# Kernel tuning notes

Hardware: AMD Instinct MI355X
Metric: run time of the kernel (lower is better)

## Reference

```python
import jax, jax.numpy as jnp
import numpy as np

# Static configuration (values of input_spatial_shapes are compile-time constants,
# mirroring how Deformable DETR fixes the FPN level sizes per image resolution).
SPATIAL_SHAPES = [(128, 128), (64, 64), (32, 32), (16, 16)]
N_HEADS = 8
N_LEVELS = 4
N_POINTS = 4
D_MODEL = 256
HEAD_DIM = D_MODEL // N_HEADS  # 32


def setup_inputs() -> dict:
    key = jax.random.key(0)
    ks = jax.random.split(key, 12)
    n = 1
    len_in = sum(h * w for h, w in SPATIAL_SHAPES)  # 21760
    len_q = len_in
    s = 0.02
    inp = {
        "query": jax.random.normal(ks[0], (n, len_q, D_MODEL), jnp.float32),
        "reference_points": jax.random.uniform(ks[1], (n, len_q, N_LEVELS, 2), jnp.float32),
        "input_flatten": jax.random.normal(ks[2], (n, len_in, D_MODEL), jnp.float32),
        "input_spatial_shapes": jnp.array(SPATIAL_SHAPES, jnp.int32),
        "input_level_start_index": jnp.array(
            np.cumsum([0] + [h * w for h, w in SPATIAL_SHAPES[:-1]]), jnp.int32
        ),
        # learned parameters (nn.Linear stores weight as [out, in])
        "W_off": jax.random.normal(ks[3], (N_HEADS * N_LEVELS * N_POINTS * 2, D_MODEL), jnp.float32) * s,
        "b_off": jax.random.normal(ks[4], (N_HEADS * N_LEVELS * N_POINTS * 2,), jnp.float32) * 0.5,
        "W_attn": jax.random.normal(ks[5], (N_HEADS * N_LEVELS * N_POINTS, D_MODEL), jnp.float32) * s,
        "b_attn": jnp.zeros((N_HEADS * N_LEVELS * N_POINTS,), jnp.float32),
        "W_val": jax.random.normal(ks[6], (D_MODEL, D_MODEL), jnp.float32) * s,
        "b_val": jnp.zeros((D_MODEL,), jnp.float32),
        "W_out": jax.random.normal(ks[7], (D_MODEL, D_MODEL), jnp.float32) * s,
        "b_out": jnp.zeros((D_MODEL,), jnp.float32),
    }
    return inp


def _bilinear_sample(img, grid, h, w):
    """torch F.grid_sample(mode='bilinear', padding_mode='zeros', align_corners=False).
    img:  [B, C, h, w]; grid: [B, Q, P, 2] in [-1, 1] -> returns [B, C, Q, P]."""
    B, C = img.shape[0], img.shape[1]
    Q, P = grid.shape[1], grid.shape[2]
    gx = (grid[..., 0] + 1.0) * (w * 0.5) - 0.5
    gy = (grid[..., 1] + 1.0) * (h * 0.5) - 0.5
    x0 = jnp.floor(gx)
    y0 = jnp.floor(gy)
    lx, ly = gx - x0, gy - y0
    x0i = x0.astype(jnp.int32)
    y0i = y0.astype(jnp.int32)
    flat = img.reshape(B, C, h * w)
    acc = jnp.zeros((B, C, Q * P), img.dtype)
    for dx, dy, wgt in (
        (0, 0, (1 - lx) * (1 - ly)),
        (1, 0, lx * (1 - ly)),
        (0, 1, (1 - lx) * ly),
        (1, 1, lx * ly),
    ):
        xi = x0i + dx
        yi = y0i + dy
        valid = (xi >= 0) & (xi < w) & (yi >= 0) & (yi < h)
        idx = (jnp.clip(yi, 0, h - 1) * w + jnp.clip(xi, 0, w - 1)).reshape(B, Q * P)
        vals = jnp.take_along_axis(flat, jnp.broadcast_to(idx[:, None, :], (B, C, Q * P)), axis=2)
        acc = acc + vals * (wgt * valid.astype(img.dtype)).reshape(B, 1, Q * P)
    return acc.reshape(B, C, Q, P)


def reference(query, reference_points, input_flatten, input_spatial_shapes,
              input_level_start_index, W_off, b_off, W_attn, b_attn,
              W_val, b_val, W_out, b_out):
    n, Q, C = query.shape
    # value projection
    value = input_flatten @ W_val.T + b_val                      # [n, Lin, C]
    value = value.reshape(n, -1, N_HEADS, HEAD_DIM)              # [n, Lin, H, D]
    # sampling offsets & attention weights from query
    off = (query @ W_off.T + b_off).reshape(n, Q, N_HEADS, N_LEVELS, N_POINTS, 2)
    aw = jax.nn.softmax(
        (query @ W_attn.T + b_attn).reshape(n, Q, N_HEADS, N_LEVELS * N_POINTS), axis=-1
    ).reshape(n, Q, N_HEADS, N_LEVELS, N_POINTS)
    # reference_points has last dim 2: normalize offsets by (w, h) per level
    norm = jnp.array([[w, h] for h, w in SPATIAL_SHAPES], jnp.float32)  # [L, 2]
    loc = reference_points[:, :, None, :, None, :] + off / norm[None, None, None, :, None, :]
    grids = 2.0 * loc - 1.0                                       # [n,Q,H,L,P,2]
    aw_t = aw.transpose(0, 2, 1, 3, 4).reshape(n * N_HEADS, 1, Q, N_LEVELS, N_POINTS)
    out = jnp.zeros((n * N_HEADS, HEAD_DIM, Q), query.dtype)
    start = 0
    for lvl, (h, w) in enumerate(SPATIAL_SHAPES):
        v = value[:, start:start + h * w]                         # [n, hw, H, D]
        start += h * w
        img = v.transpose(0, 2, 3, 1).reshape(n * N_HEADS, HEAD_DIM, h, w)
        g = grids[:, :, :, lvl].transpose(0, 2, 1, 3, 4).reshape(n * N_HEADS, Q, N_POINTS, 2)
        sampled = _bilinear_sample(img, g, h, w)                  # [nH, D, Q, P]
        out = out + (sampled * aw_t[:, :, :, lvl, :]).sum(-1)
    out = out.reshape(n, N_HEADS * HEAD_DIM, Q).transpose(0, 2, 1)  # [n, Q, C]
    return out @ W_out.T + b_out
```

## Files before the change

### kernel.cpp

```cpp
#include <hip/hip_runtime.h>
#include <math.h>

#define Q_TOTAL 21760
#define NBLK_M 340
#define QB 16
#define HEAD_IMG_BYTES 1392640

typedef _Float16     f16;
typedef short        s16x8 __attribute__((ext_vector_type(8)));
typedef f16          f16x8 __attribute__((ext_vector_type(8)));
typedef f16          f16x4 __attribute__((ext_vector_type(4)));
typedef f16          f16x2 __attribute__((ext_vector_type(2)));
typedef __bf16       bfv8  __attribute__((ext_vector_type(8)));
typedef float        f32x4 __attribute__((ext_vector_type(4)));
typedef float        f32x2 __attribute__((ext_vector_type(2)));
typedef unsigned int u32x4 __attribute__((ext_vector_type(4)));
typedef unsigned int u32x2 __attribute__((ext_vector_type(2)));

__device__ __forceinline__ s16x8 pack8(float4 a, float4 b) {
    bfv8 t;
    t[0] = (__bf16)a.x; t[1] = (__bf16)a.y; t[2] = (__bf16)a.z; t[3] = (__bf16)a.w;
    t[4] = (__bf16)b.x; t[5] = (__bf16)b.y; t[6] = (__bf16)b.z; t[7] = (__bf16)b.w;
    return __builtin_bit_cast(s16x8, t);
}

__global__ __launch_bounds__(256) void cvt_weights(
    const float* __restrict__ Woff, const float* __restrict__ Wattn,
    const float* __restrict__ Wval, const float* __restrict__ Wout,
    const float* __restrict__ boff, const float* __restrict__ battn,
    unsigned short* __restrict__ dst, float* __restrict__ bias_cat)
{
    if (blockIdx.x == 224) {
        const int t = threadIdx.x;
        bias_cat[t] = boff[t];
        if (t < 128) bias_cat[256 + t] = battn[t];
        return;
    }
    const int e = blockIdx.x * 1024 + threadIdx.x * 4;
    const float* src; int base;
    if (e < 65536)       { src = Woff;  base = 0; }
    else if (e < 98304)  { src = Wattn; base = 65536; }
    else if (e < 163840) { src = Wval;  base = 98304; }
    else                 { src = Wout;  base = 163840; }
    float4 v = *(const float4*)(src + (e - base));
    ushort4 o;
    o.x = __builtin_bit_cast(unsigned short, (__bf16)v.x);
    o.y = __builtin_bit_cast(unsigned short, (__bf16)v.y);
    o.z = __builtin_bit_cast(unsigned short, (__bf16)v.z);
    o.w = __builtin_bit_cast(unsigned short, (__bf16)v.w);
    *(ushort4*)(dst + e) = o;
}

template<bool A_BF16, int CMODE>
__global__ __launch_bounds__(256) void gemm_mfma(
    const void* __restrict__ Avoid,
    const unsigned short* __restrict__ W16,
    const float* __restrict__ bias,
    void* __restrict__ Cvoid,
    int ldc)
{
    constexpr int K = 256, BM = 64, BN = 128;
    constexpr int NB2 = BN / 2;
    constexpr int NF = NB2 / 16;
    __shared__ unsigned short As[BM * 32];
    __shared__ unsigned short Bs[BN * 32];

    const int tid  = threadIdx.x;
    const int lane = tid & 63;
    const int wv   = tid >> 6;
    const int wr   = wv >> 1, wc = wv & 1;
    const int rowBase = blockIdx.x * BM;
    const int colBase = blockIdx.y * BN;

    const int sr    = tid >> 2;
    const int skq   = (tid & 3) * 8;
    const int sslot = (tid & 3) * 16;

    f32x4 acc[2][NF];
#pragma unroll
    for (int i = 0; i < 2; i++)
#pragma unroll
        for (int j = 0; j < NF; j++) acc[i][j] = (f32x4){0.f, 0.f, 0.f, 0.f};

    const size_t arow = (size_t)(rowBase + sr) * K;

    for (int kt = 0; kt < K; kt += 32) {
        s16x8 aval;
        if constexpr (A_BF16) {
            const unsigned short* A16 = (const unsigned short*)Avoid;
            aval = *(const s16x8*)(A16 + arow + kt + skq);
        } else {
            const float* A32 = (const float*)Avoid;
            const float* p = A32 + arow + kt + skq;
            aval = pack8(*(const float4*)p, *(const float4*)(p + 4));
        }
        s16x8 bval[2];
#pragma unroll
        for (int c = 0; c < 2; c++) {
            const unsigned short* p = W16 + (size_t)(colBase + c * 64 + sr) * K + kt + skq;
            bval[c] = *(const s16x8*)p;
        }
        __syncthreads();
        *(s16x8*)(As + (((sr * 64 + sslot) ^ ((sr & 7) << 4)) >> 1)) = aval;
#pragma unroll
        for (int c = 0; c < 2; c++) {
            const int row = c * 64 + sr;
            *(s16x8*)(Bs + (((row * 64 + sslot) ^ ((row & 7) << 4)) >> 1)) = bval[c];
        }
        __syncthreads();
        s16x8 af[2];
#pragma unroll
        for (int mi = 0; mi < 2; mi++) {
            const int row = wr * 32 + mi * 16 + (lane & 15);
            af[mi] = *(const s16x8*)(As + (((row * 64 + (lane >> 4) * 16) ^ ((row & 7) << 4)) >> 1));
        }
#pragma unroll
        for (int ni = 0; ni < NF; ni++) {
            const int row = wc * NB2 + ni * 16 + (lane & 15);
            s16x8 bfrag = *(const s16x8*)(Bs + (((row * 64 + (lane >> 4) * 16) ^ ((row & 7) << 4)) >> 1));
#pragma unroll
            for (int mi = 0; mi < 2; mi++)
                acc[mi][ni] = __builtin_amdgcn_mfma_f32_16x16x32_bf16(af[mi], bfrag, acc[mi][ni], 0, 0, 0);
        }
    }

#pragma unroll
    for (int ni = 0; ni < NF; ni++) {
        const int col = colBase + wc * NB2 + ni * 16 + (lane & 15);
        const float bv = bias[col];
#pragma unroll
        for (int mi = 0; mi < 2; mi++) {
            const int r0 = rowBase + wr * 32 + mi * 16 + (lane >> 4) * 4;
#pragma unroll
            for (int j = 0; j < 4; j++) {
                const float v = acc[mi][ni][j] + bv;
                if constexpr (CMODE == 2) {
                    ((f16*)Cvoid)[((size_t)(col >> 5) * Q_TOTAL + (r0 + j)) * 32 + (col & 31)] = (f16)v;
                } else if constexpr (CMODE == 1) {
                    ((f16*)Cvoid)[(size_t)(r0 + j) * ldc + col] = (f16)v;
                } else {
                    ((float*)Cvoid)[(size_t)(r0 + j) * ldc + col] = v;
                }
            }
        }
    }
}

__global__ __launch_bounds__(256) void sample_kernel(
    const f16* __restrict__ value_t,
    const f16* __restrict__ offattn,
    const float* __restrict__ refpts,
    unsigned short* __restrict__ sampled)
{
    __shared__ __attribute__((aligned(16))) unsigned s_iw[32 * 132];

    const int tid   = threadIdx.x;
    const int qt    = blockIdx.x >> 2;
    const int hp    = blockIdx.x & 3;
    const int qbase = qt * QB;

    {
        const int q  = tid >> 4;
        const int h  = (tid >> 3) & 1;
        const int l  = (tid >> 1) & 3;
        const int ph = tid & 1;
        const int H  = hp * 2 + h;
        const int g  = tid >> 3;
        const f16* oa = offattn + (size_t)(qbase + q) * 384;

        f16x2 lgh = *(const f16x2*)(oa + 256 + H * 16 + l * 4 + ph * 2);
        const float lg0 = (float)lgh[0], lg1 = (float)lgh[1];
        float m = fmaxf(lg0, lg1);
        m = fmaxf(m, __shfl_xor(m, 1));
        m = fmaxf(m, __shfl_xor(m, 2));
        m = fmaxf(m, __shfl_xor(m, 4));
        float e0 = __expf(lg0 - m), e1 = __expf(lg1 - m);
        float s = e0 + e1;
        s += __shfl_xor(s, 1);
        s += __shfl_xor(s, 2);
        s += __shfl_xor(s, 4);
        const float inv = 1.f / s;
        const float aw2[2] = {e0 * inv, e1 * inv};

        f16x4 offh = *(const f16x4*)(oa + H * 32 + l * 8 + ph * 4);
        f32x2 rp = *(const f32x2*)(refpts + (size_t)(qbase + q) * 8 + l * 2);

        const int   SZ[4] = {128, 64, 32, 16};
        const int   ST[4] = {0, 16384, 20480, 21504};
        const int   W_ = SZ[l], START = ST[l];
        const float S = (float)W_;

        unsigned* dst = &s_iw[g * 132 + (l * 4 + ph * 2) * 8];
#pragma unroll
        for (int c = 0; c < 2; c++) {
            const float ox = (float)offh[c * 2], oy = (float)offh[c * 2 + 1];
            const float a = aw2[c];
            const float gx = fmaf(rp[0], S, ox) - 0.5f;
            const float gy = fmaf(rp[1], S, oy) - 0.5f;
            const float x0f = floorf(gx), y0f = floorf(gy);
            const float lx = gx - x0f, ly = gy - y0f;
            const int x0 = (int)x0f, y0 = (int)y0f;
            const int xs  = min(max(x0, 0), W_ - 2);
            const int sft = xs - x0;
            const float wx0 = (x0 >= 0 && x0 < W_) ? (1.f - lx) : 0.f;
            const float wx1 = (x0 + 1 >= 0 && x0 + 1 < W_) ? lx : 0.f;
            const float wxA = (sft == 0) ? wx0 : ((sft == 1) ? wx1 : 0.f);
            const float wxB = (sft == 0) ? wx1 : ((sft == -1) ? wx0 : 0.f);
            const int y1 = y0 + 1;
            const int y0c = min(max(y0, 0), W_ - 1);
            const int y1c = min(max(y1, 0), W_ - 1);
            const float wy0a = (((y0 >= 0) && (y0 < W_)) ? (1.f - ly) : 0.f) * a;
            const float wy1a = (((y1 >= 0) && (y1 < W_)) ? ly : 0.f) * a;
            const unsigned o0 = (unsigned)((START + y0c * W_ + xs) * 64);
            const unsigned o1 = (unsigned)((START + y1c * W_ + xs) * 64);
            u32x4 r0, r1;
            r0[0] = o0;      r0[1] = o1;
            r0[2] = __float_as_uint(wy0a * wxA);
            r0[3] = __float_as_uint(wy1a * wxA);
            r1[0] = o0 + 64; r1[1] = o1 + 64;
            r1[2] = __float_as_uint(wy0a * wxB);
            r1[3] = __float_as_uint(wy1a * wxB);
            *(u32x4*)(dst + c * 8)     = r0;
            *(u32x4*)(dst + c * 8 + 4) = r1;
        }
    }
    __syncthreads();

    {
        const int d8 = tid & 3;
        const int xc = (tid >> 2) & 1;
        const int g  = tid >> 3;
        const int q  = g >> 1;
        const int h  = g & 1;
        const int H  = hp * 2 + h;
        const unsigned vbase = (unsigned)(H * HEAD_IMG_BYTES) + (unsigned)(d8 * 16);
        const char* vt = (const char*)value_t;
        const unsigned* iw = &s_iw[g * 132 + xc * 4];

        float acc[8] = {0.f, 0.f, 0.f, 0.f, 0.f, 0.f, 0.f, 0.f};
#pragma unroll
        for (int half = 0; half < 2; half++) {
            u32x2 off[8];
#pragma unroll
            for (int p = 0; p < 8; p++)
                off[p] = *(const u32x2*)(iw + (half * 8 + p) * 8);
            f16x8 v0[8], v1[8];
#pragma unroll
            for (int p = 0; p < 8; p++) {
                v0[p] = *(const f16x8*)(vt + (size_t)(vbase + off[p][0]));
                v1[p] = *(const f16x8*)(vt + (size_t)(vbase + off[p][1]));
            }
#pragma unroll
            for (int p = 0; p < 8; p++) {
                const f32x2 w = *(const f32x2*)(iw + (half * 8 + p) * 8 + 2);
#pragma unroll
                for (int r = 0; r < 8; r++) {
                    acc[r] = fmaf((float)v0[p][r], w[0], acc[r]);
                    acc[r] = fmaf((float)v1[p][r], w[1], acc[r]);
                }
            }
        }
#pragma unroll
        for (int j = 0; j < 8; j++) acc[j] += __shfl_xor(acc[j], 4);

        if (xc == 0) {
            s16x8 o = pack8(make_float4(acc[0], acc[1], acc[2], acc[3]),
                            make_float4(acc[4], acc[5], acc[6], acc[7]));
            *(s16x8*)(sampled + (size_t)(qbase + q) * 256 + H * 32 + d8 * 8) = o;
        }
    }
}

extern "C" void kernel_launch(void* const* d_in, const int* in_sizes, int n_in,
                              void* d_out, int out_size, void* d_ws, size_t ws_size,
                              hipStream_t stream) {
    const float* query  = (const float*)d_in[0];
    const float* refpts = (const float*)d_in[1];
    const float* input_flatten = (const float*)d_in[2];
    const float* W_off  = (const float*)d_in[5];
    const float* b_off  = (const float*)d_in[6];
    const float* W_attn = (const float*)d_in[7];
    const float* b_attn = (const float*)d_in[8];
    const float* W_val  = (const float*)d_in[9];
    const float* b_val  = (const float*)d_in[10];
    const float* W_out  = (const float*)d_in[11];
    const float* b_out  = (const float*)d_in[12];
    float* out = (float*)d_out;

    char* ws = (char*)d_ws;
    f16*            value_t = (f16*)ws;
    f16*            offattn = (f16*)(ws + 11141120);
    unsigned short* sampled = (unsigned short*)(ws + 27852800);
    unsigned short* w16     = (unsigned short*)(ws + 38993920);
    float*          bias_cat= (float*)(ws + 39452672);
    unsigned short* w16_val  = w16 + 98304;
    unsigned short* w16_out  = w16 + 163840;

    cvt_weights<<<225, 256, 0, stream>>>(W_off, W_attn, W_val, W_out, b_off, b_attn, w16, bias_cat);

    gemm_mfma<false, 2><<<dim3(NBLK_M, 2), 256, 0, stream>>>(input_flatten, w16_val, b_val, value_t, 256);
    gemm_mfma<false, 1><<<dim3(NBLK_M, 3), 256, 0, stream>>>(query, w16, bias_cat, offattn, 384);
    sample_kernel<<<dim3((Q_TOTAL / QB) * 4), 256, 0, stream>>>(value_t, offattn, refpts, sampled);
    gemm_mfma<true, 0><<<dim3(NBLK_M, 2), 256, 0, stream>>>(sampled, w16_out, b_out, out, 256);
}
```

Measured before the change: 81.56 us.

## Fuse value and offset/attn projections into one launch, drop weight pre-conversion

Removes the separate weight-conversion kernel and instead converts fp32 weights to bf16 inline while loading each tile. The value projection and the offset/attention projection are merged into a single grid whose y-dimension selects the weight slab and output layout. Tiles grow from 64x128 to 128x128 with a 4x4 MFMA fragment grid per wave. This cuts two kernel launches and improves operand reuse, but every block now re-reads and re-converts fp32 weights, and the larger tiles raise register use and reduce the block count.

```diff
diff --git a/kernel.cpp b/kernel.cpp
--- a/kernel.cpp
+++ b/kernel.cpp
@@ -2,7 +2,6 @@
 #include <math.h>
 
 #define Q_TOTAL 21760
-#define NBLK_M 340
 #define QB 16
 #define HEAD_IMG_BYTES 1392640
 
@@ -24,124 +23,165 @@
     return __builtin_bit_cast(s16x8, t);
 }
 
-__global__ __launch_bounds__(256) void cvt_weights(
-    const float* __restrict__ Woff, const float* __restrict__ Wattn,
-    const float* __restrict__ Wval, const float* __restrict__ Wout,
-    const float* __restrict__ boff, const float* __restrict__ battn,
-    unsigned short* __restrict__ dst, float* __restrict__ bias_cat)
+__global__ __launch_bounds__(256) void gemm_fused(
+    const float* __restrict__ input_flatten,
+    const float* __restrict__ query,
+    const float* __restrict__ W_val,  const float* __restrict__ b_val,
+    const float* __restrict__ W_off,  const float* __restrict__ b_off,
+    const float* __restrict__ W_attn, const float* __restrict__ b_attn,
+    f16* __restrict__ value_t, f16* __restrict__ offattn)
 {
-    if (blockIdx.x == 224) {
-        const int t = threadIdx.x;
-        bias_cat[t] = boff[t];
-        if (t < 128) bias_cat[256 + t] = battn[t];
-        return;
-    }
-    const int e = blockIdx.x * 1024 + threadIdx.x * 4;
-    const float* src; int base;
-    if (e < 65536)       { src = Woff;  base = 0; }
-    else if (e < 98304)  { src = Wattn; base = 65536; }
-    else if (e < 163840) { src = Wval;  base = 98304; }
-    else                 { src = Wout;  base = 163840; }
-    float4 v = *(const float4*)(src + (e - base));
-    ushort4 o;
-    o.x = __builtin_bit_cast(unsigned short, (__bf16)v.x);
-    o.y = __builtin_bit_cast(unsigned short, (__bf16)v.y);
-    o.z = __builtin_bit_cast(unsigned short, (__bf16)v.z);
-    o.w = __builtin_bit_cast(unsigned short, (__bf16)v.w);
-    *(ushort4*)(dst + e) = o;
-}
-
-template<bool A_BF16, int CMODE>
-__global__ __launch_bounds__(256) void gemm_mfma(
-    const void* __restrict__ Avoid,
-    const unsigned short* __restrict__ W16,
-    const float* __restrict__ bias,
-    void* __restrict__ Cvoid,
-    int ldc)
-{
-    constexpr int K = 256, BM = 64, BN = 128;
-    constexpr int NB2 = BN / 2;
-    constexpr int NF = NB2 / 16;
-    __shared__ unsigned short As[BM * 32];
-    __shared__ unsigned short Bs[BN * 32];
+    constexpr int K = 256;
+    __shared__ unsigned short As[128 * 32];
+    __shared__ unsigned short Bs[128 * 32];
 
     const int tid  = threadIdx.x;
     const int lane = tid & 63;
     const int wv   = tid >> 6;
     const int wr   = wv >> 1, wc = wv & 1;
-    const int rowBase = blockIdx.x * BM;
-    const int colBase = blockIdx.y * BN;
-
-    const int sr    = tid >> 2;
-    const int skq   = (tid & 3) * 8;
-    const int sslot = (tid & 3) * 16;
-
-    f32x4 acc[2][NF];
-#pragma unroll
-    for (int i = 0; i < 2; i++)
-#pragma unroll
-        for (int j = 0; j < NF; j++) acc[i][j] = (f32x4){0.f, 0.f, 0.f, 0.f};
-
-    const size_t arow = (size_t)(rowBase + sr) * K;
+    const int rowBase = blockIdx.x * 128;
+    const int slab = blockIdx.y;
+
+    const float* A32; const float* Wf; const float* bias;
+    if (slab < 2)       { A32 = input_flatten; Wf = W_val + slab * 32768; bias = b_val + slab * 128; }
+    else if (slab == 2) { A32 = query;         Wf = W_off;                bias = b_off; }
+    else if (slab == 3) { A32 = query;         Wf = W_off + 32768;       bias = b_off + 128; }
+    else                { A32 = query;         Wf = W_attn;               bias = b_attn; }
+
+    const int sr  = tid >> 1;
+    const int sk0 = (tid & 1) * 16;
+    const int sby = (tid & 1) * 32;
+
+    f32x4 acc[4][4];
+#pragma unroll
+    for (int i = 0; i < 4; i++)
+#pragma unroll
+        for (int j = 0; j < 4; j++) acc[i][j] = (f32x4){0.f, 0.f, 0.f, 0.f};
+
+    const float* Ap = A32 + (size_t)(rowBase + sr) * K + sk0;
+    const float* Wp = Wf + (size_t)sr * K + sk0;
 
     for (int kt = 0; kt < K; kt += 32) {
-        s16x8 aval;
-        if constexpr (A_BF16) {
-            const unsigned short* A16 = (const unsigned short*)Avoid;
-            aval = *(const s16x8*)(A16 + arow + kt + skq);
-        } else {
-            const float* A32 = (const float*)Avoid;
-            const float* p = A32 + arow + kt + skq;
-            aval = pack8(*(const float4*)p, *(const float4*)(p + 4));
-        }
-        s16x8 bval[2];
-#pragma unroll
-        for (int c = 0; c < 2; c++) {
-            const unsigned short* p = W16 + (size_t)(colBase + c * 64 + sr) * K + kt + skq;
-            bval[c] = *(const s16x8*)p;
-        }
+        s16x8 a0 = pack8(*(const float4*)(Ap + kt),     *(const float4*)(Ap + kt + 4));
+        s16x8 a1 = pack8(*(const float4*)(Ap + kt + 8), *(const float4*)(Ap + kt + 12));
+        s16x8 b0 = pack8(*(const float4*)(Wp + kt),     *(const float4*)(Wp + kt + 4));
+        s16x8 b1 = pack8(*(const float4*)(Wp + kt + 8), *(const float4*)(Wp + kt + 12));
         __syncthreads();
-        *(s16x8*)(As + (((sr * 64 + sslot) ^ ((sr & 7) << 4)) >> 1)) = aval;
-#pragma unroll
-        for (int c = 0; c < 2; c++) {
-            const int row = c * 64 + sr;
-            *(s16x8*)(Bs + (((row * 64 + sslot) ^ ((row & 7) << 4)) >> 1)) = bval[c];
-        }
+        *(s16x8*)((char*)As + ((sr * 64 + sby)      ^ ((sr & 7) << 4))) = a0;
+        *(s16x8*)((char*)As + ((sr * 64 + sby + 16) ^ ((sr & 7) << 4))) = a1;
+        *(s16x8*)((char*)Bs + ((sr * 64 + sby)      ^ ((sr & 7) << 4))) = b0;
+        *(s16x8*)((char*)Bs + ((sr * 64 + sby + 16) ^ ((sr & 7) << 4))) = b1;
         __syncthreads();
-        s16x8 af[2];
-#pragma unroll
-        for (int mi = 0; mi < 2; mi++) {
-            const int row = wr * 32 + mi * 16 + (lane & 15);
-            af[mi] = *(const s16x8*)(As + (((row * 64 + (lane >> 4) * 16) ^ ((row & 7) << 4)) >> 1));
-        }
-#pragma unroll
-        for (int ni = 0; ni < NF; ni++) {
-            const int row = wc * NB2 + ni * 16 + (lane & 15);
-            s16x8 bfrag = *(const s16x8*)(Bs + (((row * 64 + (lane >> 4) * 16) ^ ((row & 7) << 4)) >> 1));
-#pragma unroll
-            for (int mi = 0; mi < 2; mi++)
-                acc[mi][ni] = __builtin_amdgcn_mfma_f32_16x16x32_bf16(af[mi], bfrag, acc[mi][ni], 0, 0, 0);
-        }
-    }
-
-#pragma unroll
-    for (int ni = 0; ni < NF; ni++) {
-        const int col = colBase + wc * NB2 + ni * 16 + (lane & 15);
-        const float bv = bias[col];
-#pragma unroll
-        for (int mi = 0; mi < 2; mi++) {
-            const int r0 = rowBase + wr * 32 + mi * 16 + (lane >> 4) * 4;
+        s16x8 af[4], bf[4];
+#pragma unroll
+        for (int mi = 0; mi < 4; mi++) {
+            const int row = wr * 64 + mi * 16 + (lane & 15);
+            af[mi] = *(const s16x8*)((char*)As + ((row * 64 + (lane >> 4) * 16) ^ ((row & 7) << 4)));
+        }
+#pragma unroll
+        for (int ni = 0; ni < 4; ni++) {
+            const int row = wc * 64 + ni * 16 + (lane & 15);
+            bf[ni] = *(const s16x8*)((char*)Bs + ((row * 64 + (lane >> 4) * 16) ^ ((row & 7) << 4)));
+        }
+#pragma unroll
+        for (int ni = 0; ni < 4; ni++)
+#pragma unroll
+            for (int mi = 0; mi < 4; mi++)
+                acc[mi][ni] = __builtin_amdgcn_mfma_f32_16x16x32_bf16(af[mi], bf[ni], acc[mi][ni], 0, 0, 0);
+    }
+
+#pragma unroll
+    for (int ni = 0; ni < 4; ni++) {
+        const int localcol = wc * 64 + ni * 16 + (lane & 15);
+        const float bv = bias[localcol];
+#pragma unroll
+        for (int mi = 0; mi < 4; mi++) {
+            const int r0 = rowBase + wr * 64 + mi * 16 + (lane >> 4) * 4;
 #pragma unroll
             for (int j = 0; j < 4; j++) {
                 const float v = acc[mi][ni][j] + bv;
-                if constexpr (CMODE == 2) {
-                    ((f16*)Cvoid)[((size_t)(col >> 5) * Q_TOTAL + (r0 + j)) * 32 + (col & 31)] = (f16)v;
-                } else if constexpr (CMODE == 1) {
-                    ((f16*)Cvoid)[(size_t)(r0 + j) * ldc + col] = (f16)v;
+                const int row = r0 + j;
+                if (slab < 2) {
+                    const int col = slab * 128 + localcol;
+                    value_t[((size_t)(col >> 5) * Q_TOTAL + row) * 32 + (col & 31)] = (f16)v;
                 } else {
-                    ((float*)Cvoid)[(size_t)(r0 + j) * ldc + col] = v;
+                    const int col = (slab - 2) * 128 + localcol;
+                    offattn[(size_t)row * 384 + col] = (f16)v;
                 }
             }
+        }
+    }
+}
+
+__global__ __launch_bounds__(256) void gemm_out(
+    const unsigned short* __restrict__ A16,
+    const float* __restrict__ Wf,
+    const float* __restrict__ bias,
+    float* __restrict__ C)
+{
+    constexpr int K = 256;
+    __shared__ unsigned short As[128 * 32];
+    __shared__ unsigned short Bs[128 * 32];
+
+    const int tid  = threadIdx.x;
+    const int lane = tid & 63;
+    const int wv   = tid >> 6;
+    const int wr   = wv >> 1, wc = wv & 1;
+    const int rowBase = blockIdx.x * 128;
+    const int colBase = blockIdx.y * 128;
+
+    const int sr  = tid >> 1;
+    const int sk0 = (tid & 1) * 16;
+    const int sby = (tid & 1) * 32;
+
+    f32x4 acc[4][4];
+#pragma unroll
+    for (int i = 0; i < 4; i++)
+#pragma unroll
+        for (int j = 0; j < 4; j++) acc[i][j] = (f32x4){0.f, 0.f, 0.f, 0.f};
+
+    const unsigned short* Ap = A16 + (size_t)(rowBase + sr) * K + sk0;
+    const float* Wp = Wf + (size_t)(colBase + sr) * K + sk0;
+
+    for (int kt = 0; kt < K; kt += 32) {
+        s16x8 a0 = *(const s16x8*)(Ap + kt);
+        s16x8 a1 = *(const s16x8*)(Ap + kt + 8);
+        s16x8 b0 = pack8(*(const float4*)(Wp + kt),     *(const float4*)(Wp + kt + 4));
+        s16x8 b1 = pack8(*(const float4*)(Wp + kt + 8), *(const float4*)(Wp + kt + 12));
+        __syncthreads();
+        *(s16x8*)((char*)As + ((sr * 64 + sby)      ^ ((sr & 7) << 4))) = a0;
+        *(s16x8*)((char*)As + ((sr * 64 + sby + 16) ^ ((sr & 7) << 4))) = a1;
+        *(s16x8*)((char*)Bs + ((sr * 64 + sby)      ^ ((sr & 7) << 4))) = b0;
+        *(s16x8*)((char*)Bs + ((sr * 64 + sby + 16) ^ ((sr & 7) << 4))) = b1;
+        __syncthreads();
+        s16x8 af[4], bf[4];
+#pragma unroll
+        for (int mi = 0; mi < 4; mi++) {
+            const int row = wr * 64 + mi * 16 + (lane & 15);
+            af[mi] = *(const s16x8*)((char*)As + ((row * 64 + (lane >> 4) * 16) ^ ((row & 7) << 4)));
+        }
+#pragma unroll
+        for (int ni = 0; ni < 4; ni++) {
+            const int row = wc * 64 + ni * 16 + (lane & 15);
+            bf[ni] = *(const s16x8*)((char*)Bs + ((row * 64 + (lane >> 4) * 16) ^ ((row & 7) << 4)));
+        }
+#pragma unroll
+        for (int ni = 0; ni < 4; ni++)
+#pragma unroll
+            for (int mi = 0; mi < 4; mi++)
+                acc[mi][ni] = __builtin_amdgcn_mfma_f32_16x16x32_bf16(af[mi], bf[ni], acc[mi][ni], 0, 0, 0);
+    }
+
+#pragma unroll
+    for (int ni = 0; ni < 4; ni++) {
+        const int col = colBase + wc * 64 + ni * 16 + (lane & 15);
+        const float bv = bias[col];
+#pragma unroll
+        for (int mi = 0; mi < 4; mi++) {
+            const int r0 = rowBase + wr * 64 + mi * 16 + (lane >> 4) * 4;
+#pragma unroll
+            for (int j = 0; j < 4; j++)
+                C[(size_t)(r0 + j) * 256 + col] = acc[mi][ni][j] + bv;
         }
     }
 }
@@ -291,15 +331,10 @@
     f16*            value_t = (f16*)ws;
     f16*            offattn = (f16*)(ws + 11141120);
     unsigned short* sampled = (unsigned short*)(ws + 27852800);
-    unsigned short* w16     = (unsigned short*)(ws + 38993920);
-    float*          bias_cat= (float*)(ws + 39452672);
-    unsigned short* w16_val  = w16 + 98304;
-    unsigned short* w16_out  = w16 + 163840;
-
-    cvt_weights<<<225, 256, 0, stream>>>(W_off, W_attn, W_val, W_out, b_off, b_attn, w16, bias_cat);
-
-    gemm_mfma<false, 2><<<dim3(NBLK_M, 2), 256, 0, stream>>>(input_flatten, w16_val, b_val, value_t, 256);
-    gemm_mfma<false, 1><<<dim3(NBLK_M, 3), 256, 0, stream>>>(query, w16, bias_cat, offattn, 384);
+
+    gemm_fused<<<dim3(170, 5), 256, 0, stream>>>(input_flatten, query,
+                                                 W_val, b_val, W_off, b_off, W_attn, b_attn,
+                                                 value_t, offattn);
     sample_kernel<<<dim3((Q_TOTAL / QB) * 4), 256, 0, stream>>>(value_t, offattn, refpts, sampled);
-    gemm_mfma<true, 0><<<dim3(NBLK_M, 2), 256, 0, stream>>>(sampled, w16_out, b_out, out, 256);
-}
+    gemm_out<<<dim3(170, 2), 256, 0, stream>>>(sampled, W_out, b_out, out);
+}
```

Result: slower. 84.74 us (+3.9%).
